# Performance work log

Hardware: AMD Instinct MI355X
Metric: run time of the kernel (lower is better)

The kernel has to match this reference:

```python
import jax, jax.numpy as jnp
import numpy as np

B, N, E, H = 2, 2048, 1024, 16
D = E // H  # head dim = 64


def setup_inputs() -> dict:
    key = jax.random.key(0)
    ks = jax.random.split(key, 5)
    s = 0.02
    return {
        "x": jax.random.normal(ks[0], (B, N, E), dtype=jnp.float32),
        "w_qkv": jax.random.normal(ks[1], (3 * E, E), dtype=jnp.float32) * s,
        "b_qkv": jax.random.normal(ks[2], (3 * E,), dtype=jnp.float32) * s,
        "w_proj": jax.random.normal(ks[3], (E, E), dtype=jnp.float32) * s,
        "b_proj": jax.random.normal(ks[4], (E,), dtype=jnp.float32) * s,
    }


def reference(x, w_qkv, b_qkv, w_proj, b_proj):
    # qkv projection: [B, N, 3E]
    qkv = x @ w_qkv.T + b_qkv
    # einops 'b n (h d qkv) -> qkv b h n d': qkv index is INNERMOST in the split
    qkv = qkv.reshape(B, N, H, D, 3)
    qkv = jnp.transpose(qkv, (4, 0, 2, 1, 3))  # [3, B, H, N, D]
    q, k, v = qkv[0], qkv[1], qkv[2]
    scale = 1.0 / jnp.sqrt(jnp.asarray(D, dtype=x.dtype))
    att = jnp.einsum('bhnd,bhmd->bhnm', q, k) * scale  # [B, H, N, N]
    att = jax.nn.softmax(att, axis=-1)
    out = jnp.einsum('bhnm,bhmd->bhnd', att, v)  # [B, H, N, D]
    out = jnp.transpose(out, (0, 2, 1, 3)).reshape(B, N, E)  # b n (h d)
    return out @ w_proj.T + b_proj
```

## Files before the change

### kernel.cpp

```cpp
#include <hip/hip_runtime.h>
#include <hip/hip_bf16.h>
#include <math.h>

#define B_   2
#define N_   2048
#define E_   1024
#define H_   16
#define D_   64
#define E3_  3072
#define M_   (B_ * N_)

#define QSCALE 0.18033688011112042f

using short8   = __attribute__((ext_vector_type(8))) short;
using ushort4v = __attribute__((ext_vector_type(4))) unsigned short;
using f32x4    = __attribute__((ext_vector_type(4))) float;

#define MFMA16(a, b, c) __builtin_amdgcn_mfma_f32_16x16x32_bf16((a), (b), (c), 0, 0, 0)

__device__ __forceinline__ unsigned short f2bf(float f) {
    __hip_bfloat16 h = __float2bfloat16(f);
    return __builtin_bit_cast(unsigned short, h);
}

__device__ __forceinline__ void gl16(const void* g, void* l) {
    __builtin_amdgcn_global_load_lds(
        (__attribute__((address_space(1))) const void*)g,
        (__attribute__((address_space(3))) void*)l, 16, 0, 0);
}

__global__ __launch_bounds__(256) void convert_kernel(
    const float* __restrict__ x, const float* __restrict__ wq,
    const float* __restrict__ wp,
    unsigned short* __restrict__ xb, unsigned short* __restrict__ wqp,
    unsigned short* __restrict__ wpb)
{
    const int o = (blockIdx.x * 256 + threadIdx.x) * 8;
    const float* src;
    unsigned short* dst;
    if (o < 4194304) {
        src = x + o; dst = xb + o;
    } else if (o < 7340032) {
        const int oo = o - 4194304;
        const int s = oo >> 10, k = oo & 1023;
        const int c = s >> 10, rem = s & 1023;
        const int h = rem >> 6, d = rem & 63;
        src = wq + (size_t)(h * 192 + d * 3 + c) * E_ + k;
        dst = wqp + oo;
    } else {
        const int oo = o - 7340032;
        src = wp + oo; dst = wpb + oo;
    }
    float4 a = *(const float4*)src;
    float4 b = *(const float4*)(src + 4);
    short8 r;
    r[0] = (short)f2bf(a.x); r[1] = (short)f2bf(a.y);
    r[2] = (short)f2bf(a.z); r[3] = (short)f2bf(a.w);
    r[4] = (short)f2bf(b.x); r[5] = (short)f2bf(b.y);
    r[6] = (short)f2bf(b.z); r[7] = (short)f2bf(b.w);
    *(short8*)dst = r;
}

#define GEMM_STAGE(Aglob, Bglob)                                            \
    {                                                                        \
        _Pragma("unroll")                                                    \
        for (int i2 = 0; i2 < 2; ++i2) {                                     \
            const int chunk = wv * 128 + i2 * 64 + lane;                     \
            const int row = chunk >> 2;                                      \
            const int gcg = (chunk & 3) ^ ((row >> 1) & 3);                  \
            const int lbase = (wv * 128 + i2 * 64) * 8;                      \
            gl16(Aglob + (size_t)(bm + row) * E_ + k0 + gcg * 8, &As[lbase]);\
            gl16(Bglob + (size_t)(bn + row) * E_ + k0 + gcg * 8, &Bs[lbase]);\
        }                                                                    \
    }

#define GEMM_COMPUTE()                                                       \
    {                                                                        \
        const int sw = (l15 >> 1) & 3;                                       \
        short8 af[4], bf[4];                                                 \
        _Pragma("unroll")                                                    \
        for (int i = 0; i < 4; ++i) {                                        \
            const int ra = wr * 64 + i * 16 + l15;                           \
            const int rb = wc * 64 + i * 16 + l15;                           \
            af[i] = *(const short8*)&As[ra * 32 + (quad ^ sw) * 8];          \
            bf[i] = *(const short8*)&Bs[rb * 32 + (quad ^ sw) * 8];          \
        }                                                                    \
        _Pragma("unroll")                                                    \
        for (int i = 0; i < 4; ++i)                                          \
            _Pragma("unroll")                                                \
            for (int j = 0; j < 4; ++j)                                      \
                acc[i][j] = MFMA16(af[i], bf[j], acc[i][j]);                 \
    }

__global__ __launch_bounds__(256) void qkv_kernel(
    const unsigned short* __restrict__ A, const unsigned short* __restrict__ Bm,
    const float* __restrict__ bias,
    unsigned short* __restrict__ Q, unsigned short* __restrict__ K,
    unsigned short* __restrict__ VT)
{
    __shared__ __attribute__((aligned(16))) unsigned short As[128 * 32];
    __shared__ __attribute__((aligned(16))) unsigned short Bs[128 * 32];
    const int t    = threadIdx.x;
    const int wv   = t >> 6, lane = t & 63;
    const int quad = lane >> 4, l15 = lane & 15;
    const int wr   = wv & 1, wc = wv >> 1;
    const int bm   = blockIdx.y * 128, bn = blockIdx.x * 128;

    f32x4 acc[4][4];
#pragma unroll
    for (int i = 0; i < 4; ++i)
#pragma unroll
        for (int j = 0; j < 4; ++j) acc[i][j] = (f32x4){0.f, 0.f, 0.f, 0.f};

    for (int k0 = 0; k0 < E_; k0 += 32) {
        __syncthreads();
        GEMM_STAGE(A, Bm);
        __syncthreads();
        GEMM_COMPUTE();
    }

    const int c = bn >> 10;
#pragma unroll
    for (int j = 0; j < 4; ++j) {
        const int s   = bn + wc * 64 + j * 16 + l15;
        const int rem = s & 1023;
        const int h   = rem >> 6, d = rem & 63;
        const float bcol = bias[h * 192 + d * 3 + c];
#pragma unroll
        for (int i = 0; i < 4; ++i) {
            const int row0 = bm + wr * 64 + i * 16 + quad * 4;
            const int b    = row0 >> 11;
            const int n0   = row0 & (N_ - 1);
            if (c == 0) {
#pragma unroll
                for (int g = 0; g < 4; ++g)
                    Q[(((size_t)b * H_ + h) * N_ + n0 + g) * D_ + d] =
                        f2bf((acc[i][j][g] + bcol) * QSCALE);
            } else if (c == 1) {
#pragma unroll
                for (int g = 0; g < 4; ++g)
                    K[(((size_t)b * H_ + h) * N_ + n0 + g) * D_ + d] =
                        f2bf(acc[i][j][g] + bcol);
            } else {
                ushort4v pk;
#pragma unroll
                for (int g = 0; g < 4; ++g) pk[g] = f2bf(acc[i][j][g] + bcol);
                *(ushort4v*)&VT[(((size_t)b * H_ + h) * D_ + d) * N_ + n0] = pk;
            }
        }
    }
}

__global__ __launch_bounds__(256) void attn_kernel(
    const unsigned short* __restrict__ Q, const unsigned short* __restrict__ K,
    const unsigned short* __restrict__ VT, unsigned short* __restrict__ CTX)
{
    __shared__ __attribute__((aligned(16))) __hip_bfloat16 Qs[64][72];
    __shared__ __attribute__((aligned(16))) __hip_bfloat16 Ks[64][72];
    __shared__ __attribute__((aligned(16))) __hip_bfloat16 Vs[64][72];
    __shared__ __attribute__((aligned(16))) __hip_bfloat16 Ps[4][16][72];

    const int t    = threadIdx.x;
    const int wv   = t >> 6, lane = t & 63;
    const int quad = lane >> 4, l15 = lane & 15;
    const int qt   = blockIdx.x & 31;
    const int bh   = blockIdx.x >> 5;
    const int r0   = t >> 3, c8 = (t & 7) * 8;

    const unsigned short* Qp = Q + ((size_t)bh * N_ + qt * 64) * D_;
    const unsigned short* Kp = K + (size_t)bh * N_ * D_;
    const unsigned short* Vp = VT + (size_t)bh * D_ * N_;

#pragma unroll
    for (int p = 0; p < 2; ++p) {
        const int rr = r0 + p * 32;
        *(short8*)&Qs[rr][c8] = *(const short8*)(Qp + rr * D_ + c8);
    }

    f32x4 O[4];
#pragma unroll
    for (int i = 0; i < 4; ++i) O[i] = (f32x4){0.f, 0.f, 0.f, 0.f};
    float lsum[4] = {0.f, 0.f, 0.f, 0.f};

    __syncthreads();

    for (int kt = 0; kt < N_ / 64; ++kt) {
#pragma unroll
        for (int p = 0; p < 2; ++p) {
            const int rr = r0 + p * 32;
            *(short8*)&Ks[rr][c8] = *(const short8*)(Kp + (size_t)(kt * 64 + rr) * D_ + c8);
            *(short8*)&Vs[rr][c8] = *(const short8*)(Vp + (size_t)rr * N_ + kt * 64 + c8);
        }
        __syncthreads();

        f32x4 st[4];
#pragma unroll
        for (int i = 0; i < 4; ++i) st[i] = (f32x4){0.f, 0.f, 0.f, 0.f};
#pragma unroll
        for (int ks = 0; ks < 2; ++ks) {
            short8 aq = *(const short8*)&Qs[wv * 16 + l15][ks * 32 + quad * 8];
#pragma unroll
            for (int nt = 0; nt < 4; ++nt) {
                short8 bk = *(const short8*)&Ks[nt * 16 + l15][ks * 32 + quad * 8];
                st[nt] = MFMA16(aq, bk, st[nt]);
            }
        }

#pragma unroll
        for (int nt = 0; nt < 4; ++nt)
#pragma unroll
            for (int g = 0; g < 4; ++g) {
                const float p = exp2f(st[nt][g]);
                lsum[g] += p;
                Ps[wv][quad * 4 + g][nt * 16 + l15] = __float2bfloat16(p);
            }

#pragma unroll
        for (int ks = 0; ks < 2; ++ks) {
            short8 ap = *(const short8*)&Ps[wv][l15][ks * 32 + quad * 8];
#pragma unroll
            for (int nt = 0; nt < 4; ++nt) {
                short8 bv = *(const short8*)&Vs[nt * 16 + l15][ks * 32 + quad * 8];
                O[nt] = MFMA16(ap, bv, O[nt]);
            }
        }
        __syncthreads();
    }

#pragma unroll
    for (int off = 1; off < 16; off <<= 1)
#pragma unroll
        for (int g = 0; g < 4; ++g)
            lsum[g] += __shfl_xor(lsum[g], off, 64);

    const int b = bh >> 4;
    const int h = bh & 15;
#pragma unroll
    for (int g = 0; g < 4; ++g) {
        const float inv = 1.0f / lsum[g];
        const int qrow  = qt * 64 + wv * 16 + quad * 4 + g;
#pragma unroll
        for (int nt = 0; nt < 4; ++nt)
            CTX[((size_t)b * N_ + qrow) * E_ + h * D_ + nt * 16 + l15] =
                f2bf(O[nt][g] * inv);
    }
}

__global__ __launch_bounds__(256) void proj_kernel(
    const unsigned short* __restrict__ A, const unsigned short* __restrict__ Bm,
    const float* __restrict__ bias, float* __restrict__ out)
{
    __shared__ __attribute__((aligned(16))) unsigned short As[128 * 32];
    __shared__ __attribute__((aligned(16))) unsigned short Bs[128 * 32];
    const int t    = threadIdx.x;
    const int wv   = t >> 6, lane = t & 63;
    const int quad = lane >> 4, l15 = lane & 15;
    const int wr   = wv & 1, wc = wv >> 1;
    const int bm   = blockIdx.y * 128, bn = blockIdx.x * 128;

    f32x4 acc[4][4];
#pragma unroll
    for (int i = 0; i < 4; ++i)
#pragma unroll
        for (int j = 0; j < 4; ++j) acc[i][j] = (f32x4){0.f, 0.f, 0.f, 0.f};

    for (int k0 = 0; k0 < E_; k0 += 32) {
        __syncthreads();
        GEMM_STAGE(A, Bm);
        __syncthreads();
        GEMM_COMPUTE();
    }

#pragma unroll
    for (int j = 0; j < 4; ++j) {
        const int col = bn + wc * 64 + j * 16 + l15;
        const float bcol = bias[col];
#pragma unroll
        for (int i = 0; i < 4; ++i) {
#pragma unroll
            for (int g = 0; g < 4; ++g) {
                const int row = bm + wr * 64 + i * 16 + quad * 4 + g;
                out[(size_t)row * E_ + col] = acc[i][j][g] + bcol;
            }
        }
    }
}

extern "C" void kernel_launch(void* const* d_in, const int* in_sizes, int n_in,
                              void* d_out, int out_size, void* d_ws, size_t ws_size,
                              hipStream_t stream)
{
    const float* x      = (const float*)d_in[0];
    const float* w_qkv  = (const float*)d_in[1];
    const float* b_qkv  = (const float*)d_in[2];
    const float* w_proj = (const float*)d_in[3];
    const float* b_proj = (const float*)d_in[4];
    float* out = (float*)d_out;

    unsigned short* xb  = (unsigned short*)d_ws;
    unsigned short* wqp = xb  + 4194304;
    unsigned short* wpb = wqp + 3145728;
    unsigned short* Q   = wpb + 1048576;
    unsigned short* K   = Q   + 4194304;
    unsigned short* VT  = K   + 4194304;
    unsigned short* CTX = VT  + 4194304;

    dim3 blk(256);
    convert_kernel<<<dim3(4096), blk, 0, stream>>>(x, w_qkv, w_proj, xb, wqp, wpb);

    dim3 g1(E3_ / 128, M_ / 128);
    qkv_kernel<<<g1, blk, 0, stream>>>(xb, wqp, b_qkv, Q, K, VT);

    dim3 g2(B_ * H_ * (N_ / 64));
    attn_kernel<<<g2, blk, 0, stream>>>(Q, K, VT, CTX);

    dim3 g3(E_ / 128, M_ / 128);
    proj_kernel<<<g3, blk, 0, stream>>>(CTX, w_proj ? wpb : wpb, b_proj, out);
}
```

Baseline: 219.1 us.

## Transpose GEMM fragments for vectorized epilogues, register-resident Q, split QKV kernel

Swaps the MFMA operand order in the Q/K and projection GEMMs so each lane holds four consecutive output columns. This allows packed bf16 and float4 stores in place of scattered scalar writes. Attention now computes S^T with K as the A operand and keeps Q fragments in registers, which removes the Q shared tile. It also writes P with packed stores, uses the hardware exp2, and reduces row sums with a single cross-lane shuffle pass. The QKV GEMM is split into separate Q/K and V kernels, and a pre-permuted, pre-scaled bias is built in an extra convert block. Rounding now uses a manual add-and-truncate bf16 conversion that does not handle NaN, and the QKV work needs one extra kernel launch.

Result: no change. 219.0 us (-0.0%).

```diff
diff --git a/kernel.cpp b/kernel.cpp
--- a/kernel.cpp
+++ b/kernel.cpp
@@ -12,15 +12,33 @@
 
 #define QSCALE 0.18033688011112042f
 
-using short8   = __attribute__((ext_vector_type(8))) short;
-using ushort4v = __attribute__((ext_vector_type(4))) unsigned short;
-using f32x4    = __attribute__((ext_vector_type(4))) float;
+using short8 = __attribute__((ext_vector_type(8))) short;
+using f32x4  = __attribute__((ext_vector_type(4))) float;
+using uint2v = __attribute__((ext_vector_type(2))) unsigned int;
 
 #define MFMA16(a, b, c) __builtin_amdgcn_mfma_f32_16x16x32_bf16((a), (b), (c), 0, 0, 0)
 
 __device__ __forceinline__ unsigned short f2bf(float f) {
     __hip_bfloat16 h = __float2bfloat16(f);
     return __builtin_bit_cast(unsigned short, h);
+}
+
+__device__ __forceinline__ float fast_exp2(float x) {
+#if __has_builtin(__builtin_amdgcn_exp2f)
+    return __builtin_amdgcn_exp2f(x);
+#else
+    return exp2f(x);
+#endif
+}
+
+__device__ __forceinline__ unsigned int pack_bf16_rh(float lo, float hi) {
+    unsigned int ulo = __builtin_bit_cast(unsigned int, lo) + 0x8000u;
+    unsigned int uhi = __builtin_bit_cast(unsigned int, hi) + 0x8000u;
+#if __has_builtin(__builtin_amdgcn_perm)
+    return __builtin_amdgcn_perm(uhi, ulo, 0x07060302u);
+#else
+    return (uhi & 0xFFFF0000u) | (ulo >> 16);
+#endif
 }
 
 __device__ __forceinline__ void gl16(const void* g, void* l) {
@@ -31,10 +49,20 @@
 
 __global__ __launch_bounds__(256) void convert_kernel(
     const float* __restrict__ x, const float* __restrict__ wq,
-    const float* __restrict__ wp,
+    const float* __restrict__ wp, const float* __restrict__ b_qkv,
     unsigned short* __restrict__ xb, unsigned short* __restrict__ wqp,
-    unsigned short* __restrict__ wpb)
-{
+    unsigned short* __restrict__ wpb, float* __restrict__ bias_perm)
+{
+    if (blockIdx.x == 4096) {
+        for (int q = threadIdx.x; q < E3_; q += 256) {
+            const int c = q >> 10, rem = q & 1023;
+            const int h = rem >> 6, d = rem & 63;
+            float v = b_qkv[h * 192 + d * 3 + c];
+            if (c == 0) v *= QSCALE;
+            bias_perm[q] = v;
+        }
+        return;
+    }
     const int o = (blockIdx.x * 256 + threadIdx.x) * 8;
     const float* src;
     unsigned short* dst;
@@ -53,15 +81,14 @@
     }
     float4 a = *(const float4*)src;
     float4 b = *(const float4*)(src + 4);
-    short8 r;
-    r[0] = (short)f2bf(a.x); r[1] = (short)f2bf(a.y);
-    r[2] = (short)f2bf(a.z); r[3] = (short)f2bf(a.w);
-    r[4] = (short)f2bf(b.x); r[5] = (short)f2bf(b.y);
-    r[6] = (short)f2bf(b.z); r[7] = (short)f2bf(b.w);
-    *(short8*)dst = r;
-}
-
-#define GEMM_STAGE(Aglob, Bglob)                                            \
+    uint2v p0, p1;
+    p0.x = pack_bf16_rh(a.x, a.y); p0.y = pack_bf16_rh(a.z, a.w);
+    p1.x = pack_bf16_rh(b.x, b.y); p1.y = pack_bf16_rh(b.z, b.w);
+    *(uint2v*)dst = p0;
+    *(uint2v*)(dst + 4) = p1;
+}
+
+#define GEMM_STAGE(Aglob, Bglob)                                             \
     {                                                                        \
         _Pragma("unroll")                                                    \
         for (int i2 = 0; i2 < 2; ++i2) {                                     \
@@ -74,7 +101,7 @@
         }                                                                    \
     }
 
-#define GEMM_COMPUTE()                                                       \
+#define GEMM_COMPUTE(MARR, NARR)                                             \
     {                                                                        \
         const int sw = (l15 >> 1) & 3;                                       \
         short8 af[4], bf[4];                                                 \
@@ -82,8 +109,8 @@
         for (int i = 0; i < 4; ++i) {                                        \
             const int ra = wr * 64 + i * 16 + l15;                           \
             const int rb = wc * 64 + i * 16 + l15;                           \
-            af[i] = *(const short8*)&As[ra * 32 + (quad ^ sw) * 8];          \
-            bf[i] = *(const short8*)&Bs[rb * 32 + (quad ^ sw) * 8];          \
+            af[i] = *(const short8*)&MARR[ra * 32 + ((quad ^ sw) * 8)];      \
+            bf[i] = *(const short8*)&NARR[rb * 32 + ((quad ^ sw) * 8)];      \
         }                                                                    \
         _Pragma("unroll")                                                    \
         for (int i = 0; i < 4; ++i)                                          \
@@ -92,61 +119,94 @@
                 acc[i][j] = MFMA16(af[i], bf[j], acc[i][j]);                 \
     }
 
-__global__ __launch_bounds__(256) void qkv_kernel(
+#define GEMM_PROLOG                                                          \
+    const int t    = threadIdx.x;                                            \
+    const int wv   = t >> 6, lane = t & 63;                                  \
+    const int quad = lane >> 4, l15 = lane & 15;                             \
+    const int wr   = wv & 1, wc = wv >> 1;                                   \
+    f32x4 acc[4][4];                                                         \
+    _Pragma("unroll")                                                        \
+    for (int i = 0; i < 4; ++i)                                              \
+        _Pragma("unroll")                                                    \
+        for (int j = 0; j < 4; ++j) acc[i][j] = (f32x4){0.f, 0.f, 0.f, 0.f};
+
+__global__ __launch_bounds__(256) void qkv_qk_kernel(
     const unsigned short* __restrict__ A, const unsigned short* __restrict__ Bm,
-    const float* __restrict__ bias,
-    unsigned short* __restrict__ Q, unsigned short* __restrict__ K,
-    unsigned short* __restrict__ VT)
+    const float* __restrict__ bias_perm,
+    unsigned short* __restrict__ Q, unsigned short* __restrict__ K)
 {
     __shared__ __attribute__((aligned(16))) unsigned short As[128 * 32];
     __shared__ __attribute__((aligned(16))) unsigned short Bs[128 * 32];
-    const int t    = threadIdx.x;
-    const int wv   = t >> 6, lane = t & 63;
-    const int quad = lane >> 4, l15 = lane & 15;
-    const int wr   = wv & 1, wc = wv >> 1;
-    const int bm   = blockIdx.y * 128, bn = blockIdx.x * 128;
-
-    f32x4 acc[4][4];
-#pragma unroll
-    for (int i = 0; i < 4; ++i)
-#pragma unroll
-        for (int j = 0; j < 4; ++j) acc[i][j] = (f32x4){0.f, 0.f, 0.f, 0.f};
+    GEMM_PROLOG
+    const int bm = blockIdx.y * 128;
+    const int bn = blockIdx.x * 128;
 
     for (int k0 = 0; k0 < E_; k0 += 32) {
         __syncthreads();
         GEMM_STAGE(A, Bm);
         __syncthreads();
-        GEMM_COMPUTE();
+        GEMM_COMPUTE(Bs, As);
     }
 
     const int c = bn >> 10;
+    const float scale = (c == 0) ? QSCALE : 1.0f;
+    unsigned short* dst0 = (c == 0) ? Q : K;
+#pragma unroll
+    for (int i = 0; i < 4; ++i) {
+        const int s0 = bn + wr * 64 + i * 16 + quad * 4;
+        const int h  = (s0 >> 6) & 15;
+        const int d0 = s0 & 63;
+        const float4 bq = *(const float4*)(bias_perm + s0);
+#pragma unroll
+        for (int j = 0; j < 4; ++j) {
+            const int row = bm + wc * 64 + j * 16 + l15;
+            const int b   = row >> 11, n = row & (N_ - 1);
+            const float v0 = fmaf(acc[i][j][0], scale, bq.x);
+            const float v1 = fmaf(acc[i][j][1], scale, bq.y);
+            const float v2 = fmaf(acc[i][j][2], scale, bq.z);
+            const float v3 = fmaf(acc[i][j][3], scale, bq.w);
+            uint2v pk;
+            pk.x = pack_bf16_rh(v0, v1);
+            pk.y = pack_bf16_rh(v2, v3);
+            *(uint2v*)(dst0 + (((size_t)b * H_ + h) * N_ + n) * D_ + d0) = pk;
+        }
+    }
+}
+
+__global__ __launch_bounds__(256) void qkv_v_kernel(
+    const unsigned short* __restrict__ A, const unsigned short* __restrict__ Bm,
+    const float* __restrict__ bias_perm, unsigned short* __restrict__ VT)
+{
+    __shared__ __attribute__((aligned(16))) unsigned short As[128 * 32];
+    __shared__ __attribute__((aligned(16))) unsigned short Bs[128 * 32];
+    GEMM_PROLOG
+    const int bm = blockIdx.y * 128;
+    const int bn = 2048 + blockIdx.x * 128;
+
+    for (int k0 = 0; k0 < E_; k0 += 32) {
+        __syncthreads();
+        GEMM_STAGE(A, Bm);
+        __syncthreads();
+        GEMM_COMPUTE(As, Bs);
+    }
+
 #pragma unroll
     for (int j = 0; j < 4; ++j) {
-        const int s   = bn + wc * 64 + j * 16 + l15;
-        const int rem = s & 1023;
-        const int h   = rem >> 6, d = rem & 63;
-        const float bcol = bias[h * 192 + d * 3 + c];
+        const int s = bn + wc * 64 + j * 16 + l15;
+        const int h = (s >> 6) & 15, d = s & 63;
+        const float bv = bias_perm[s];
 #pragma unroll
         for (int i = 0; i < 4; ++i) {
             const int row0 = bm + wr * 64 + i * 16 + quad * 4;
-            const int b    = row0 >> 11;
-            const int n0   = row0 & (N_ - 1);
-            if (c == 0) {
-#pragma unroll
-                for (int g = 0; g < 4; ++g)
-                    Q[(((size_t)b * H_ + h) * N_ + n0 + g) * D_ + d] =
-                        f2bf((acc[i][j][g] + bcol) * QSCALE);
-            } else if (c == 1) {
-#pragma unroll
-                for (int g = 0; g < 4; ++g)
-                    K[(((size_t)b * H_ + h) * N_ + n0 + g) * D_ + d] =
-                        f2bf(acc[i][j][g] + bcol);
-            } else {
-                ushort4v pk;
-#pragma unroll
-                for (int g = 0; g < 4; ++g) pk[g] = f2bf(acc[i][j][g] + bcol);
-                *(ushort4v*)&VT[(((size_t)b * H_ + h) * D_ + d) * N_ + n0] = pk;
-            }
+            const int b    = row0 >> 11, n0 = row0 & (N_ - 1);
+            const float v0 = acc[i][j][0] + bv;
+            const float v1 = acc[i][j][1] + bv;
+            const float v2 = acc[i][j][2] + bv;
+            const float v3 = acc[i][j][3] + bv;
+            uint2v pk;
+            pk.x = pack_bf16_rh(v0, v1);
+            pk.y = pack_bf16_rh(v2, v3);
+            *(uint2v*)(VT + (((size_t)b * H_ + h) * D_ + d) * N_ + n0) = pk;
         }
     }
 }
@@ -155,10 +215,9 @@
     const unsigned short* __restrict__ Q, const unsigned short* __restrict__ K,
     const unsigned short* __restrict__ VT, unsigned short* __restrict__ CTX)
 {
-    __shared__ __attribute__((aligned(16))) __hip_bfloat16 Qs[64][72];
-    __shared__ __attribute__((aligned(16))) __hip_bfloat16 Ks[64][72];
-    __shared__ __attribute__((aligned(16))) __hip_bfloat16 Vs[64][72];
-    __shared__ __attribute__((aligned(16))) __hip_bfloat16 Ps[4][16][72];
+    __shared__ __attribute__((aligned(16))) unsigned short Ks[64 * 72];
+    __shared__ __attribute__((aligned(16))) unsigned short Vs[64 * 72];
+    __shared__ __attribute__((aligned(16))) unsigned short Ps[4][16 * 72];
 
     const int t    = threadIdx.x;
     const int wv   = t >> 6, lane = t & 63;
@@ -167,77 +226,75 @@
     const int bh   = blockIdx.x >> 5;
     const int r0   = t >> 3, c8 = (t & 7) * 8;
 
-    const unsigned short* Qp = Q + ((size_t)bh * N_ + qt * 64) * D_;
     const unsigned short* Kp = K + (size_t)bh * N_ * D_;
     const unsigned short* Vp = VT + (size_t)bh * D_ * N_;
-
-#pragma unroll
-    for (int p = 0; p < 2; ++p) {
-        const int rr = r0 + p * 32;
-        *(short8*)&Qs[rr][c8] = *(const short8*)(Qp + rr * D_ + c8);
-    }
+    const unsigned short* Qp = Q + ((size_t)bh * N_ + qt * 64 + wv * 16 + l15) * D_;
+
+    const short8 qf0 = *(const short8*)(Qp + quad * 8);
+    const short8 qf1 = *(const short8*)(Qp + 32 + quad * 8);
 
     f32x4 O[4];
 #pragma unroll
     for (int i = 0; i < 4; ++i) O[i] = (f32x4){0.f, 0.f, 0.f, 0.f};
-    float lsum[4] = {0.f, 0.f, 0.f, 0.f};
-
-    __syncthreads();
+    f32x4 lsum4 = {0.f, 0.f, 0.f, 0.f};
 
     for (int kt = 0; kt < N_ / 64; ++kt) {
 #pragma unroll
         for (int p = 0; p < 2; ++p) {
             const int rr = r0 + p * 32;
-            *(short8*)&Ks[rr][c8] = *(const short8*)(Kp + (size_t)(kt * 64 + rr) * D_ + c8);
-            *(short8*)&Vs[rr][c8] = *(const short8*)(Vp + (size_t)rr * N_ + kt * 64 + c8);
+            *(short8*)&Ks[rr * 72 + c8] =
+                *(const short8*)(Kp + (size_t)(kt * 64 + rr) * D_ + c8);
+            *(short8*)&Vs[rr * 72 + c8] =
+                *(const short8*)(Vp + (size_t)rr * N_ + kt * 64 + c8);
         }
         __syncthreads();
 
         f32x4 st[4];
 #pragma unroll
-        for (int i = 0; i < 4; ++i) st[i] = (f32x4){0.f, 0.f, 0.f, 0.f};
+        for (int kb = 0; kb < 4; ++kb) st[kb] = (f32x4){0.f, 0.f, 0.f, 0.f};
+#pragma unroll
+        for (int kb = 0; kb < 4; ++kb) {
+            const int krow = (kb * 16 + l15) * 72;
+            const short8 kf0 = *(const short8*)&Ks[krow + quad * 8];
+            const short8 kf1 = *(const short8*)&Ks[krow + 32 + quad * 8];
+            st[kb] = MFMA16(kf0, qf0, st[kb]);
+            st[kb] = MFMA16(kf1, qf1, st[kb]);
+        }
+
+#pragma unroll
+        for (int kb = 0; kb < 4; ++kb) {
+            f32x4 pv;
+#pragma unroll
+            for (int g = 0; g < 4; ++g) pv[g] = fast_exp2(st[kb][g]);
+            lsum4 += pv;
+            uint2v pk;
+            pk.x = pack_bf16_rh(pv[0], pv[1]);
+            pk.y = pack_bf16_rh(pv[2], pv[3]);
+            *(uint2v*)&Ps[wv][l15 * 72 + kb * 16 + quad * 4] = pk;
+        }
+
 #pragma unroll
         for (int ks = 0; ks < 2; ++ks) {
-            short8 aq = *(const short8*)&Qs[wv * 16 + l15][ks * 32 + quad * 8];
+            const short8 pf = *(const short8*)&Ps[wv][l15 * 72 + ks * 32 + quad * 8];
 #pragma unroll
             for (int nt = 0; nt < 4; ++nt) {
-                short8 bk = *(const short8*)&Ks[nt * 16 + l15][ks * 32 + quad * 8];
-                st[nt] = MFMA16(aq, bk, st[nt]);
+                const short8 vf =
+                    *(const short8*)&Vs[(nt * 16 + l15) * 72 + ks * 32 + quad * 8];
+                O[nt] = MFMA16(pf, vf, O[nt]);
             }
         }
-
-#pragma unroll
-        for (int nt = 0; nt < 4; ++nt)
-#pragma unroll
-            for (int g = 0; g < 4; ++g) {
-                const float p = exp2f(st[nt][g]);
-                lsum[g] += p;
-                Ps[wv][quad * 4 + g][nt * 16 + l15] = __float2bfloat16(p);
-            }
-
-#pragma unroll
-        for (int ks = 0; ks < 2; ++ks) {
-            short8 ap = *(const short8*)&Ps[wv][l15][ks * 32 + quad * 8];
-#pragma unroll
-            for (int nt = 0; nt < 4; ++nt) {
-                short8 bv = *(const short8*)&Vs[nt * 16 + l15][ks * 32 + quad * 8];
-                O[nt] = MFMA16(ap, bv, O[nt]);
-            }
-        }
-        __syncthreads();
-    }
-
-#pragma unroll
-    for (int off = 1; off < 16; off <<= 1)
-#pragma unroll
-        for (int g = 0; g < 4; ++g)
-            lsum[g] += __shfl_xor(lsum[g], off, 64);
-
-    const int b = bh >> 4;
-    const int h = bh & 15;
+        __syncthreads();
+    }
+
+    float lt = lsum4[0] + lsum4[1] + lsum4[2] + lsum4[3];
+    lt += __shfl_xor(lt, 16, 64);
+    lt += __shfl_xor(lt, 32, 64);
+
+    const int b = bh >> 4, h = bh & 15;
 #pragma unroll
     for (int g = 0; g < 4; ++g) {
-        const float inv = 1.0f / lsum[g];
+        const float lg  = __shfl(lt, quad * 4 + g, 64);
+        const float inv = 1.0f / lg;
         const int qrow  = qt * 64 + wv * 16 + quad * 4 + g;
 #pragma unroll
         for (int nt = 0; nt < 4; ++nt)
@@ -252,36 +309,30 @@
 {
     __shared__ __attribute__((aligned(16))) unsigned short As[128 * 32];
     __shared__ __attribute__((aligned(16))) unsigned short Bs[128 * 32];
-    const int t    = threadIdx.x;
-    const int wv   = t >> 6, lane = t & 63;
-    const int quad = lane >> 4, l15 = lane & 15;
-    const int wr   = wv & 1, wc = wv >> 1;
-    const int bm   = blockIdx.y * 128, bn = blockIdx.x * 128;
-
-    f32x4 acc[4][4];
-#pragma unroll
-    for (int i = 0; i < 4; ++i)
-#pragma unroll
-        for (int j = 0; j < 4; ++j) acc[i][j] = (f32x4){0.f, 0.f, 0.f, 0.f};
+    GEMM_PROLOG
+    const int bm = blockIdx.y * 128;
+    const int bn = blockIdx.x * 128;
 
     for (int k0 = 0; k0 < E_; k0 += 32) {
         __syncthreads();
         GEMM_STAGE(A, Bm);
         __syncthreads();
-        GEMM_COMPUTE();
-    }
-
-#pragma unroll
-    for (int j = 0; j < 4; ++j) {
-        const int col = bn + wc * 64 + j * 16 + l15;
-        const float bcol = bias[col];
-#pragma unroll
-        for (int i = 0; i < 4; ++i) {
-#pragma unroll
-            for (int g = 0; g < 4; ++g) {
-                const int row = bm + wr * 64 + i * 16 + quad * 4 + g;
-                out[(size_t)row * E_ + col] = acc[i][j][g] + bcol;
-            }
+        GEMM_COMPUTE(Bs, As);
+    }
+
+#pragma unroll
+    for (int i = 0; i < 4; ++i) {
+        const int col0 = bn + wr * 64 + i * 16 + quad * 4;
+        const float4 bp = *(const float4*)(bias + col0);
+#pragma unroll
+        for (int j = 0; j < 4; ++j) {
+            const int row = bm + wc * 64 + j * 16 + l15;
+            float4 o;
+            o.x = acc[i][j][0] + bp.x;
+            o.y = acc[i][j][1] + bp.y;
+            o.z = acc[i][j][2] + bp.z;
+            o.w = acc[i][j][3] + bp.w;
+            *(float4*)(out + (size_t)row * E_ + col0) = o;
         }
     }
 }
@@ -304,16 +355,16 @@
     unsigned short* K   = Q   + 4194304;
     unsigned short* VT  = K   + 4194304;
     unsigned short* CTX = VT  + 4194304;
+    float* bias_perm    = (float*)(CTX + 4194304);
 
     dim3 blk(256);
-    convert_kernel<<<dim3(4096), blk, 0, stream>>>(x, w_qkv, w_proj, xb, wqp, wpb);
-
-    dim3 g1(E3_ / 128, M_ / 128);
-    qkv_kernel<<<g1, blk, 0, stream>>>(xb, wqp, b_qkv, Q, K, VT);
-
-    dim3 g2(B_ * H_ * (N_ / 64));
-    attn_kernel<<<g2, blk, 0, stream>>>(Q, K, VT, CTX);
-
-    dim3 g3(E_ / 128, M_ / 128);
-    proj_kernel<<<g3, blk, 0, stream>>>(CTX, w_proj ? wpb : wpb, b_proj, out);
-}
+    convert_kernel<<<dim3(4097), blk, 0, stream>>>(
+        x, w_qkv, w_proj, b_qkv, xb, wqp, wpb, bias_perm);
+
+    qkv_qk_kernel<<<dim3(16, 32), blk, 0, stream>>>(xb, wqp, bias_perm, Q, K);
+    qkv_v_kernel<<<dim3(8, 32), blk, 0, stream>>>(xb, wqp, bias_perm, VT);
+
+    attn_kernel<<<dim3(B_ * H_ * (N_ / 64)), blk, 0, stream>>>(Q, K, VT, CTX);
+
+    proj_kernel<<<dim3(8, 32), blk, 0, stream>>>(CTX, wpb, b_proj, out);
+}
```
